# Kernel optimization log

Hardware: AMD Instinct MI355X
Metric: run time of the kernel (lower is better)

## Reference

```python
import jax, jax.numpy as jnp
import numpy as np
import math

BSZ, SEQLEN, DIM = 16, 1, 4096
N_HEADS, N_KV_HEADS = 32, 8
HEAD_DIM = DIM // N_HEADS  # 128
MAX_SEQ_LEN = 4096
START_POS = 4095


def setup_inputs() -> dict:
    key = jax.random.key(0)
    ks = jax.random.split(key, 8)
    w_scale = 0.02
    x = jax.random.normal(ks[0], (1, BSZ, SEQLEN, DIM), jnp.float32)
    wq = jax.random.normal(ks[1], (DIM, DIM), jnp.float32) * w_scale
    wk = jax.random.normal(ks[2], (N_KV_HEADS * HEAD_DIM, DIM), jnp.float32) * w_scale
    wv = jax.random.normal(ks[3], (N_KV_HEADS * HEAD_DIM, DIM), jnp.float32) * w_scale
    wo = jax.random.normal(ks[4], (DIM, DIM), jnp.float32) * w_scale
    cache_k = jax.random.normal(ks[5], (BSZ, MAX_SEQ_LEN, N_KV_HEADS, HEAD_DIM), jnp.float32)
    cache_v = jax.random.normal(ks[6], (BSZ, MAX_SEQ_LEN, N_KV_HEADS, HEAD_DIM), jnp.float32)
    # real RoPE frequencies for positions [START_POS, START_POS+SEQLEN)
    inv_freq = 1.0 / (10000.0 ** (np.arange(0, HEAD_DIM, 2, dtype=np.float32) / HEAD_DIM))
    pos = np.arange(START_POS, START_POS + SEQLEN, dtype=np.float32)
    ang = pos[:, None] * inv_freq[None, :]  # [seqlen, head_dim/2]
    freqs_cos = jnp.asarray(np.cos(ang), jnp.float32)
    freqs_sin = jnp.asarray(np.sin(ang), jnp.float32)
    return {"x": x, "wq": wq, "wk": wk, "wv": wv, "wo": wo,
            "cache_k": cache_k, "cache_v": cache_v,
            "freqs_cos": freqs_cos, "freqs_sin": freqs_sin,
            "start_pos": START_POS}


def _apply_rope(t, cos, sin):
    # t: [b, s, h, d]; cos/sin: [s, d/2]; complex mult over interleaved pairs
    b, s, h, d = t.shape
    tr = t.reshape(b, s, h, d // 2, 2)
    a, bb = tr[..., 0], tr[..., 1]
    c = cos[None, :, None, :]
    sn = sin[None, :, None, :]
    out = jnp.stack([a * c - bb * sn, a * sn + bb * c], axis=-1)
    return out.reshape(b, s, h, d)


def reference(x, wq, wk, wv, wo, cache_k, cache_v, freqs_cos, freqs_sin, start_pos):
    _, bsz, seqlen, dim = x.shape
    n_kv_heads, head_dim = cache_k.shape[2], cache_k.shape[3]
    n_heads = dim // head_dim
    n_rep = n_heads // n_kv_heads

    xq = jnp.einsum('obsd,ed->obse', x, wq).reshape(bsz, seqlen, n_heads, head_dim)
    xk = jnp.einsum('obsd,ed->obse', x, wk).reshape(bsz, seqlen, n_kv_heads, head_dim)
    xv = jnp.einsum('obsd,ed->obse', x, wv).reshape(bsz, seqlen, n_kv_heads, head_dim)

    xq = _apply_rope(xq, freqs_cos, freqs_sin)
    xk = _apply_rope(xk, freqs_cos, freqs_sin)

    cache_k = cache_k.at[:, start_pos:start_pos + seqlen].set(xk)
    cache_v = cache_v.at[:, start_pos:start_pos + seqlen].set(xv)
    keys = cache_k[:, :start_pos + seqlen]    # [b, L, kvh, hd]
    values = cache_v[:, :start_pos + seqlen]

    # repeat_kv (GQA expansion)
    keys = jnp.repeat(keys, n_rep, axis=2)     # [b, L, h, hd]
    values = jnp.repeat(values, n_rep, axis=2)

    scale = 1.0 / math.sqrt(head_dim)
    scores = jnp.einsum('bqhd,bkhd->bhqk', xq, keys) * scale
    # mask is None in decode (seqlen == 1)
    attn = jax.nn.softmax(scores, axis=-1)
    out = jnp.einsum('bhqk,bkhd->bqhd', attn, values)
    out = out.reshape(1, bsz, seqlen, dim)
    return jnp.einsum('obsd,ed->obse', out, wo)
```

## Files before the change

### kernel.cpp

```cpp
#include <hip/hip_runtime.h>
#include <math.h>

#define BSZ 16
#define DIMM 4096
#define NKVH 8
#define HD 128
#define SEQ 4096
#define NSPLIT 8
#define SPLITLEN 512
#define RPAD 65

__device__ __forceinline__ void gemv_rows(const float* __restrict__ xg,
                                          const float* __restrict__ W,
                                          int rbase,
                                          float* __restrict__ x_lds,
                                          float* __restrict__ rbuf,
                                          float res[4], int tid) {
  const int lane = tid & 63;
  float acc[4][16];
#pragma unroll
  for (int r = 0; r < 4; ++r)
#pragma unroll
    for (int b = 0; b < 16; ++b) acc[r][b] = 0.f;

  for (int c = 0; c < 16; ++c) {
    __syncthreads();
#pragma unroll
    for (int u = 0; u < 4; ++u) {
      int f = u * 256 + tid;
      int b = f >> 6;
      int dl = (f & 63) << 2;
      ((float4*)x_lds)[f] = *(const float4*)(xg + (size_t)b * DIMM + c * 256 + dl);
    }
    __syncthreads();
    float4 w4[4];
#pragma unroll
    for (int r = 0; r < 4; ++r)
      w4[r] = *(const float4*)(W + (size_t)(rbase + r) * DIMM + c * 256 + (lane << 2));
#pragma unroll
    for (int b = 0; b < 16; ++b) {
      float4 xv = ((const float4*)x_lds)[b * 64 + lane];
#pragma unroll
      for (int r = 0; r < 4; ++r) {
        acc[r][b] = fmaf(w4[r].x, xv.x, acc[r][b]);
        acc[r][b] = fmaf(w4[r].y, xv.y, acc[r][b]);
        acc[r][b] = fmaf(w4[r].z, xv.z, acc[r][b]);
        acc[r][b] = fmaf(w4[r].w, xv.w, acc[r][b]);
      }
    }
  }
#pragma unroll
  for (int r = 0; r < 4; ++r) {
    __syncthreads();
#pragma unroll
    for (int b = 0; b < 16; ++b) rbuf[b * RPAD + lane] = acc[r][b];
    __syncthreads();
    int bb = lane >> 2, j = lane & 3;
    float s = 0.f;
#pragma unroll
    for (int k = 0; k < 16; ++k) s += rbuf[bb * RPAD + j * 16 + k];
    s += __shfl_xor(s, 1);
    s += __shfl_xor(s, 2);
    res[r] = s;
  }
}

__global__ __launch_bounds__(256) void qkv_kernel(
    const float* __restrict__ x, const float* __restrict__ wq,
    const float* __restrict__ wk, const float* __restrict__ wv,
    const float* __restrict__ fcos, const float* __restrict__ fsin,
    float* __restrict__ q_ws, float* __restrict__ k_ws, float* __restrict__ v_ws) {
  __shared__ float x_lds[4096];
  __shared__ float red[4][16 * RPAD];
  const int tid = threadIdx.x;
  const int lane = tid & 63;
  const int wave = tid >> 6;
  const int row0 = blockIdx.x * 16 + wave * 4;

  const float* W;
  float* outp;
  int rbase, ostride;
  bool rope;
  if (row0 < 4096)      { W = wq; rbase = row0;        outp = q_ws; rope = true;  ostride = 4096; }
  else if (row0 < 5120) { W = wk; rbase = row0 - 4096; outp = k_ws; rope = true;  ostride = 1024; }
  else                  { W = wv; rbase = row0 - 5120; outp = v_ws; rope = false; ostride = 1024; }

  float res[4];
  gemv_rows(x, W, rbase, x_lds, red[wave], res, tid);

  if (rope) {
    int pos = rbase & 127;
#pragma unroll
    for (int r = 0; r < 4; r += 2) {
      int i = (pos + r) >> 1;
      float c = fcos[i], s = fsin[i];
      float a = res[r], b2 = res[r + 1];
      res[r]     = a * c - b2 * s;
      res[r + 1] = a * s + b2 * c;
    }
  }
  if ((lane & 3) == 0) {
    int b = lane >> 2;
#pragma unroll
    for (int r = 0; r < 4; ++r) outp[(size_t)b * ostride + rbase + r] = res[r];
  }
}

__global__ __launch_bounds__(256) void attn_kernel(
    const float* __restrict__ ck, const float* __restrict__ cv,
    const float* __restrict__ q_ws, const float* __restrict__ k_new,
    const float* __restrict__ v_new, float* __restrict__ ml_ws,
    float* __restrict__ opart) {
  __shared__ float sc[SPLITLEN * 4];
  __shared__ float part[16 * 128];
  const int tid = threadIdx.x, lane = tid & 63, wave = tid >> 6;
  const int split = blockIdx.x, kvh = blockIdx.y, b = blockIdx.z;
  const int p0 = split * SPLITLEN;
  const float scale = 0.08838834764831845f;

  const int dsub = (lane & 7) << 2;
  const int prow = lane >> 3;
  float4 q4[4][4];
#pragma unroll
  for (int h = 0; h < 4; ++h)
#pragma unroll
    for (int j = 0; j < 4; ++j) {
      float4 t = *(const float4*)(q_ws + (size_t)b * 4096 + (kvh * 4 + h) * 128 + j * 32 + dsub);
      q4[h][j] = make_float4(t.x * scale, t.y * scale, t.z * scale, t.w * scale);
    }

  for (int it = 0; it < 16; ++it) {
    int p = p0 + wave * 128 + it * 8 + prow;
    const float* kp = (p == 4095) ? (k_new + (size_t)(b * 8 + kvh) * 128)
                                  : (ck + ((size_t)(b * 4096 + p) * 8 + kvh) * 128);
    float s0 = 0, s1 = 0, s2 = 0, s3 = 0;
#pragma unroll
    for (int j = 0; j < 4; ++j) {
      float4 k4 = *(const float4*)(kp + j * 32 + dsub);
      s0 = fmaf(k4.x, q4[0][j].x, s0); s0 = fmaf(k4.y, q4[0][j].y, s0);
      s0 = fmaf(k4.z, q4[0][j].z, s0); s0 = fmaf(k4.w, q4[0][j].w, s0);
      s1 = fmaf(k4.x, q4[1][j].x, s1); s1 = fmaf(k4.y, q4[1][j].y, s1);
      s1 = fmaf(k4.z, q4[1][j].z, s1); s1 = fmaf(k4.w, q4[1][j].w, s1);
      s2 = fmaf(k4.x, q4[2][j].x, s2); s2 = fmaf(k4.y, q4[2][j].y, s2);
      s2 = fmaf(k4.z, q4[2][j].z, s2); s2 = fmaf(k4.w, q4[2][j].w, s2);
      s3 = fmaf(k4.x, q4[3][j].x, s3); s3 = fmaf(k4.y, q4[3][j].y, s3);
      s3 = fmaf(k4.z, q4[3][j].z, s3); s3 = fmaf(k4.w, q4[3][j].w, s3);
    }
#pragma unroll
    for (int m = 1; m <= 4; m <<= 1) {
      s0 += __shfl_xor(s0, m); s1 += __shfl_xor(s1, m);
      s2 += __shfl_xor(s2, m); s3 += __shfl_xor(s3, m);
    }
    if ((lane & 7) == 0)
      ((float4*)sc)[wave * 128 + it * 8 + prow] = make_float4(s0, s1, s2, s3);
  }
  __syncthreads();

  {
    int h = wave;
    float vals[8];
    float m = -1e30f;
#pragma unroll
    for (int k = 0; k < 8; ++k) {
      vals[k] = sc[(k * 64 + lane) * 4 + h];
      m = fmaxf(m, vals[k]);
    }
#pragma unroll
    for (int mk = 1; mk <= 32; mk <<= 1) m = fmaxf(m, __shfl_xor(m, mk));
    float lsum = 0;
#pragma unroll
    for (int k = 0; k < 8; ++k) {
      float e = __expf(vals[k] - m);
      sc[(k * 64 + lane) * 4 + h] = e;
      lsum += e;
    }
#pragma unroll
    for (int mk = 1; mk <= 32; mk <<= 1) lsum += __shfl_xor(lsum, mk);
    if (lane == 0) {
      int hg = kvh * 4 + h;
      ml_ws[((size_t)(b * 32 + hg) * NSPLIT + split) * 2 + 0] = m;
      ml_ws[((size_t)(b * 32 + hg) * NSPLIT + split) * 2 + 1] = lsum;
    }
  }
  __syncthreads();

  {
    int d0 = lane * 2;
    float a00 = 0, a01 = 0, a10 = 0, a11 = 0, a20 = 0, a21 = 0, a30 = 0, a31 = 0;
    for (int k = 0; k < 128; ++k) {
      int pl = wave * 128 + k;
      int p = p0 + pl;
      const float* vp = (p == 4095) ? (v_new + (size_t)(b * 8 + kvh) * 128)
                                    : (cv + ((size_t)(b * 4096 + p) * 8 + kvh) * 128);
      float2 v2 = *(const float2*)(vp + d0);
      float4 s4 = ((const float4*)sc)[pl];
      a00 = fmaf(s4.x, v2.x, a00); a01 = fmaf(s4.x, v2.y, a01);
      a10 = fmaf(s4.y, v2.x, a10); a11 = fmaf(s4.y, v2.y, a11);
      a20 = fmaf(s4.z, v2.x, a20); a21 = fmaf(s4.z, v2.y, a21);
      a30 = fmaf(s4.w, v2.x, a30); a31 = fmaf(s4.w, v2.y, a31);
    }
    *(float2*)&part[(wave * 4 + 0) * 128 + d0] = make_float2(a00, a01);
    *(float2*)&part[(wave * 4 + 1) * 128 + d0] = make_float2(a10, a11);
    *(float2*)&part[(wave * 4 + 2) * 128 + d0] = make_float2(a20, a21);
    *(float2*)&part[(wave * 4 + 3) * 128 + d0] = make_float2(a30, a31);
  }
  __syncthreads();
  {
    int hh = tid >> 6, dd = (tid & 63) * 2;
    float o0 = 0, o1 = 0;
#pragma unroll
    for (int w = 0; w < 4; ++w) {
      o0 += part[(w * 4 + hh) * 128 + dd];
      o1 += part[(w * 4 + hh) * 128 + dd + 1];
    }
    int hg = kvh * 4 + hh;
    size_t base = ((size_t)(b * 32 + hg) * NSPLIT + split) * 128;
    *(float2*)(opart + base + dd) = make_float2(o0, o1);
  }
}

__global__ __launch_bounds__(128) void combine_kernel(
    const float* __restrict__ ml_ws, const float* __restrict__ opart,
    float* __restrict__ attn_ws) {
  int bh = blockIdx.x;
  int d = threadIdx.x;
  float mv[NSPLIT], lv[NSPLIT];
  float M = -1e30f;
#pragma unroll
  for (int i = 0; i < NSPLIT; ++i) {
    mv[i] = ml_ws[((size_t)bh * NSPLIT + i) * 2];
    lv[i] = ml_ws[((size_t)bh * NSPLIT + i) * 2 + 1];
    M = fmaxf(M, mv[i]);
  }
  float L = 0, o = 0;
#pragma unroll
  for (int i = 0; i < NSPLIT; ++i) {
    float w = __expf(mv[i] - M);
    L += w * lv[i];
    o += w * opart[((size_t)bh * NSPLIT + i) * 128 + d];
  }
  attn_ws[(size_t)bh * 128 + d] = o / L;
}

__global__ __launch_bounds__(256) void oproj_kernel(
    const float* __restrict__ xin, const float* __restrict__ wo,
    float* __restrict__ out) {
  __shared__ float x_lds[4096];
  __shared__ float red[4][16 * RPAD];
  const int tid = threadIdx.x;
  const int lane = tid & 63;
  const int wave = tid >> 6;
  const int row0 = blockIdx.x * 16 + wave * 4;
  float res[4];
  gemv_rows(xin, wo, row0, x_lds, red[wave], res, tid);
  if ((lane & 3) == 0) {
    int b = lane >> 2;
#pragma unroll
    for (int r = 0; r < 4; ++r) out[(size_t)b * 4096 + row0 + r] = res[r];
  }
}

extern "C" void kernel_launch(void* const* d_in, const int* in_sizes, int n_in,
                              void* d_out, int out_size, void* d_ws, size_t ws_size,
                              hipStream_t stream) {
  const float* x  = (const float*)d_in[0];
  const float* wq = (const float*)d_in[1];
  const float* wk = (const float*)d_in[2];
  const float* wv = (const float*)d_in[3];
  const float* wo = (const float*)d_in[4];
  const float* ck = (const float*)d_in[5];
  const float* cv = (const float*)d_in[6];
  const float* fc = (const float*)d_in[7];
  const float* fs = (const float*)d_in[8];

  float* ws      = (float*)d_ws;
  float* q_ws    = ws;
  float* k_ws    = q_ws + 65536;
  float* v_ws    = k_ws + 16384;
  float* ml_ws   = v_ws + 16384;
  float* opart   = ml_ws + 8192;
  float* attn_ws = opart + 524288;

  qkv_kernel<<<384, 256, 0, stream>>>(x, wq, wk, wv, fc, fs, q_ws, k_ws, v_ws);
  attn_kernel<<<dim3(NSPLIT, NKVH, BSZ), 256, 0, stream>>>(ck, cv, q_ws, k_ws, v_ws,
                                                           ml_ws, opart);
  combine_kernel<<<BSZ * 32, 128, 0, stream>>>(ml_ws, opart, attn_ws);
  oproj_kernel<<<256, 256, 0, stream>>>(attn_ws, wo, (float*)d_out);
}
```

Baseline: 674.8 us.

## Double grid parallelism in GEMVs and attention splits, write new KV into cache

Halves rows per wave in the QKV and output-projection GEMVs so twice as many blocks run, and doubles the number of KV splits in attention with shorter per-block ranges. The new K/V rows are written directly into the input cache at the last position, removing the per-position branch in the attention loops. The PV accumulation switches to float4 loads over two position halves. This trades more partial results and combine work, plus in-place mutation of input buffers, for higher occupancy and parallelism.

```diff
diff --git a/kernel.cpp b/kernel.cpp
--- a/kernel.cpp
+++ b/kernel.cpp
@@ -6,20 +6,20 @@
 #define NKVH 8
 #define HD 128
 #define SEQ 4096
-#define NSPLIT 8
-#define SPLITLEN 512
+#define NSPLIT 16
+#define SPLITLEN 256
 #define RPAD 65
 
-__device__ __forceinline__ void gemv_rows(const float* __restrict__ xg,
-                                          const float* __restrict__ W,
-                                          int rbase,
-                                          float* __restrict__ x_lds,
-                                          float* __restrict__ rbuf,
-                                          float res[4], int tid) {
+__device__ __forceinline__ void gemv_rows2(const float* __restrict__ xg,
+                                           const float* __restrict__ W,
+                                           int rbase,
+                                           float* __restrict__ x_lds,
+                                           float* __restrict__ rbuf,
+                                           float res[2], int tid) {
   const int lane = tid & 63;
-  float acc[4][16];
-#pragma unroll
-  for (int r = 0; r < 4; ++r)
+  float acc[2][16];
+#pragma unroll
+  for (int r = 0; r < 2; ++r)
 #pragma unroll
     for (int b = 0; b < 16; ++b) acc[r][b] = 0.f;
 
@@ -33,15 +33,15 @@
       ((float4*)x_lds)[f] = *(const float4*)(xg + (size_t)b * DIMM + c * 256 + dl);
     }
     __syncthreads();
-    float4 w4[4];
-#pragma unroll
-    for (int r = 0; r < 4; ++r)
+    float4 w4[2];
+#pragma unroll
+    for (int r = 0; r < 2; ++r)
       w4[r] = *(const float4*)(W + (size_t)(rbase + r) * DIMM + c * 256 + (lane << 2));
 #pragma unroll
     for (int b = 0; b < 16; ++b) {
       float4 xv = ((const float4*)x_lds)[b * 64 + lane];
 #pragma unroll
-      for (int r = 0; r < 4; ++r) {
+      for (int r = 0; r < 2; ++r) {
         acc[r][b] = fmaf(w4[r].x, xv.x, acc[r][b]);
         acc[r][b] = fmaf(w4[r].y, xv.y, acc[r][b]);
         acc[r][b] = fmaf(w4[r].z, xv.z, acc[r][b]);
@@ -50,7 +50,7 @@
     }
   }
 #pragma unroll
-  for (int r = 0; r < 4; ++r) {
+  for (int r = 0; r < 2; ++r) {
     __syncthreads();
 #pragma unroll
     for (int b = 0; b < 16; ++b) rbuf[b * RPAD + lane] = acc[r][b];
@@ -69,99 +69,101 @@
     const float* __restrict__ x, const float* __restrict__ wq,
     const float* __restrict__ wk, const float* __restrict__ wv,
     const float* __restrict__ fcos, const float* __restrict__ fsin,
-    float* __restrict__ q_ws, float* __restrict__ k_ws, float* __restrict__ v_ws) {
+    float* __restrict__ q_ws, float* __restrict__ ckw, float* __restrict__ cvw) {
   __shared__ float x_lds[4096];
   __shared__ float red[4][16 * RPAD];
   const int tid = threadIdx.x;
   const int lane = tid & 63;
   const int wave = tid >> 6;
-  const int row0 = blockIdx.x * 16 + wave * 4;
+  const int row0 = blockIdx.x * 8 + wave * 2;
 
   const float* W;
-  float* outp;
-  int rbase, ostride;
-  bool rope;
-  if (row0 < 4096)      { W = wq; rbase = row0;        outp = q_ws; rope = true;  ostride = 4096; }
-  else if (row0 < 5120) { W = wk; rbase = row0 - 4096; outp = k_ws; rope = true;  ostride = 1024; }
-  else                  { W = wv; rbase = row0 - 5120; outp = v_ws; rope = false; ostride = 1024; }
-
-  float res[4];
-  gemv_rows(x, W, rbase, x_lds, red[wave], res, tid);
-
-  if (rope) {
-    int pos = rbase & 127;
-#pragma unroll
-    for (int r = 0; r < 4; r += 2) {
-      int i = (pos + r) >> 1;
-      float c = fcos[i], s = fsin[i];
-      float a = res[r], b2 = res[r + 1];
-      res[r]     = a * c - b2 * s;
-      res[r + 1] = a * s + b2 * c;
-    }
+  int rbase, kind;
+  if (row0 < 4096)      { W = wq; rbase = row0;        kind = 0; }
+  else if (row0 < 5120) { W = wk; rbase = row0 - 4096; kind = 1; }
+  else                  { W = wv; rbase = row0 - 5120; kind = 2; }
+
+  float res[2];
+  gemv_rows2(x, W, rbase, x_lds, red[wave], res, tid);
+
+  if (kind <= 1) {
+    int i = (rbase & 127) >> 1;
+    float c = fcos[i], s = fsin[i];
+    float a = res[0], b2 = res[1];
+    res[0] = a * c - b2 * s;
+    res[1] = a * s + b2 * c;
   }
   if ((lane & 3) == 0) {
     int b = lane >> 2;
-#pragma unroll
-    for (int r = 0; r < 4; ++r) outp[(size_t)b * ostride + rbase + r] = res[r];
+    if (kind == 0) {
+#pragma unroll
+      for (int r = 0; r < 2; ++r) q_ws[(size_t)b * 4096 + rbase + r] = res[r];
+    } else {
+      int kvh = rbase >> 7, dpos = rbase & 127;
+      float* dst = (kind == 1) ? ckw : cvw;
+#pragma unroll
+      for (int r = 0; r < 2; ++r)
+        dst[((size_t)(b * 4096 + 4095) * 8 + kvh) * 128 + dpos + r] = res[r];
+    }
   }
 }
 
 __global__ __launch_bounds__(256) void attn_kernel(
     const float* __restrict__ ck, const float* __restrict__ cv,
-    const float* __restrict__ q_ws, const float* __restrict__ k_new,
-    const float* __restrict__ v_new, float* __restrict__ ml_ws,
+    const float* __restrict__ q_ws, float* __restrict__ ml_ws,
     float* __restrict__ opart) {
   __shared__ float sc[SPLITLEN * 4];
-  __shared__ float part[16 * 128];
+  __shared__ float part[32 * 128];
   const int tid = threadIdx.x, lane = tid & 63, wave = tid >> 6;
   const int split = blockIdx.x, kvh = blockIdx.y, b = blockIdx.z;
   const int p0 = split * SPLITLEN;
   const float scale = 0.08838834764831845f;
 
-  const int dsub = (lane & 7) << 2;
-  const int prow = lane >> 3;
-  float4 q4[4][4];
-#pragma unroll
-  for (int h = 0; h < 4; ++h)
-#pragma unroll
-    for (int j = 0; j < 4; ++j) {
-      float4 t = *(const float4*)(q_ws + (size_t)b * 4096 + (kvh * 4 + h) * 128 + j * 32 + dsub);
-      q4[h][j] = make_float4(t.x * scale, t.y * scale, t.z * scale, t.w * scale);
-    }
-
-  for (int it = 0; it < 16; ++it) {
-    int p = p0 + wave * 128 + it * 8 + prow;
-    const float* kp = (p == 4095) ? (k_new + (size_t)(b * 8 + kvh) * 128)
-                                  : (ck + ((size_t)(b * 4096 + p) * 8 + kvh) * 128);
-    float s0 = 0, s1 = 0, s2 = 0, s3 = 0;
-#pragma unroll
-    for (int j = 0; j < 4; ++j) {
-      float4 k4 = *(const float4*)(kp + j * 32 + dsub);
-      s0 = fmaf(k4.x, q4[0][j].x, s0); s0 = fmaf(k4.y, q4[0][j].y, s0);
-      s0 = fmaf(k4.z, q4[0][j].z, s0); s0 = fmaf(k4.w, q4[0][j].w, s0);
-      s1 = fmaf(k4.x, q4[1][j].x, s1); s1 = fmaf(k4.y, q4[1][j].y, s1);
-      s1 = fmaf(k4.z, q4[1][j].z, s1); s1 = fmaf(k4.w, q4[1][j].w, s1);
-      s2 = fmaf(k4.x, q4[2][j].x, s2); s2 = fmaf(k4.y, q4[2][j].y, s2);
-      s2 = fmaf(k4.z, q4[2][j].z, s2); s2 = fmaf(k4.w, q4[2][j].w, s2);
-      s3 = fmaf(k4.x, q4[3][j].x, s3); s3 = fmaf(k4.y, q4[3][j].y, s3);
-      s3 = fmaf(k4.z, q4[3][j].z, s3); s3 = fmaf(k4.w, q4[3][j].w, s3);
-    }
-#pragma unroll
-    for (int m = 1; m <= 4; m <<= 1) {
-      s0 += __shfl_xor(s0, m); s1 += __shfl_xor(s1, m);
-      s2 += __shfl_xor(s2, m); s3 += __shfl_xor(s3, m);
-    }
-    if ((lane & 7) == 0)
-      ((float4*)sc)[wave * 128 + it * 8 + prow] = make_float4(s0, s1, s2, s3);
+  {
+    const int dsub = (lane & 7) << 2;
+    const int prow = lane >> 3;
+    float4 q4[4][4];
+#pragma unroll
+    for (int h = 0; h < 4; ++h)
+#pragma unroll
+      for (int j = 0; j < 4; ++j) {
+        float4 t = *(const float4*)(q_ws + (size_t)b * 4096 + (kvh * 4 + h) * 128 + j * 32 + dsub);
+        q4[h][j] = make_float4(t.x * scale, t.y * scale, t.z * scale, t.w * scale);
+      }
+#pragma unroll 2
+    for (int it = 0; it < 8; ++it) {
+      int pl = wave * 64 + it * 8 + prow;
+      const float* kp = ck + ((size_t)(b * 4096 + p0 + pl) * 8 + kvh) * 128;
+      float s0 = 0, s1 = 0, s2 = 0, s3 = 0;
+#pragma unroll
+      for (int j = 0; j < 4; ++j) {
+        float4 k4 = *(const float4*)(kp + j * 32 + dsub);
+        s0 = fmaf(k4.x, q4[0][j].x, s0); s0 = fmaf(k4.y, q4[0][j].y, s0);
+        s0 = fmaf(k4.z, q4[0][j].z, s0); s0 = fmaf(k4.w, q4[0][j].w, s0);
+        s1 = fmaf(k4.x, q4[1][j].x, s1); s1 = fmaf(k4.y, q4[1][j].y, s1);
+        s1 = fmaf(k4.z, q4[1][j].z, s1); s1 = fmaf(k4.w, q4[1][j].w, s1);
+        s2 = fmaf(k4.x, q4[2][j].x, s2); s2 = fmaf(k4.y, q4[2][j].y, s2);
+        s2 = fmaf(k4.z, q4[2][j].z, s2); s2 = fmaf(k4.w, q4[2][j].w, s2);
+        s3 = fmaf(k4.x, q4[3][j].x, s3); s3 = fmaf(k4.y, q4[3][j].y, s3);
+        s3 = fmaf(k4.z, q4[3][j].z, s3); s3 = fmaf(k4.w, q4[3][j].w, s3);
+      }
+#pragma unroll
+      for (int m = 1; m <= 4; m <<= 1) {
+        s0 += __shfl_xor(s0, m); s1 += __shfl_xor(s1, m);
+        s2 += __shfl_xor(s2, m); s3 += __shfl_xor(s3, m);
+      }
+      if ((lane & 7) == 0)
+        ((float4*)sc)[pl] = make_float4(s0, s1, s2, s3);
+    }
   }
   __syncthreads();
 
   {
     int h = wave;
-    float vals[8];
+    float vals[4];
     float m = -1e30f;
 #pragma unroll
-    for (int k = 0; k < 8; ++k) {
+    for (int k = 0; k < 4; ++k) {
       vals[k] = sc[(k * 64 + lane) * 4 + h];
       m = fmaxf(m, vals[k]);
     }
@@ -169,7 +171,7 @@
     for (int mk = 1; mk <= 32; mk <<= 1) m = fmaxf(m, __shfl_xor(m, mk));
     float lsum = 0;
 #pragma unroll
-    for (int k = 0; k < 8; ++k) {
+    for (int k = 0; k < 4; ++k) {
       float e = __expf(vals[k] - m);
       sc[(k * 64 + lane) * 4 + h] = e;
       lsum += e;
@@ -185,33 +187,39 @@
   __syncthreads();
 
   {
-    int d0 = lane * 2;
-    float a00 = 0, a01 = 0, a10 = 0, a11 = 0, a20 = 0, a21 = 0, a30 = 0, a31 = 0;
-    for (int k = 0; k < 128; ++k) {
-      int pl = wave * 128 + k;
-      int p = p0 + pl;
-      const float* vp = (p == 4095) ? (v_new + (size_t)(b * 8 + kvh) * 128)
-                                    : (cv + ((size_t)(b * 4096 + p) * 8 + kvh) * 128);
-      float2 v2 = *(const float2*)(vp + d0);
+    const int dq = lane & 31;
+    const int half = lane >> 5;
+    float4 a0 = {0,0,0,0}, a1 = {0,0,0,0}, a2 = {0,0,0,0}, a3 = {0,0,0,0};
+#pragma unroll 4
+    for (int it = 0; it < 32; ++it) {
+      int pl = wave * 64 + it * 2 + half;
+      const float* vp = cv + ((size_t)(b * 4096 + p0 + pl) * 8 + kvh) * 128;
+      float4 v4 = *(const float4*)(vp + dq * 4);
       float4 s4 = ((const float4*)sc)[pl];
-      a00 = fmaf(s4.x, v2.x, a00); a01 = fmaf(s4.x, v2.y, a01);
-      a10 = fmaf(s4.y, v2.x, a10); a11 = fmaf(s4.y, v2.y, a11);
-      a20 = fmaf(s4.z, v2.x, a20); a21 = fmaf(s4.z, v2.y, a21);
-      a30 = fmaf(s4.w, v2.x, a30); a31 = fmaf(s4.w, v2.y, a31);
-    }
-    *(float2*)&part[(wave * 4 + 0) * 128 + d0] = make_float2(a00, a01);
-    *(float2*)&part[(wave * 4 + 1) * 128 + d0] = make_float2(a10, a11);
-    *(float2*)&part[(wave * 4 + 2) * 128 + d0] = make_float2(a20, a21);
-    *(float2*)&part[(wave * 4 + 3) * 128 + d0] = make_float2(a30, a31);
+      a0.x = fmaf(s4.x, v4.x, a0.x); a0.y = fmaf(s4.x, v4.y, a0.y);
+      a0.z = fmaf(s4.x, v4.z, a0.z); a0.w = fmaf(s4.x, v4.w, a0.w);
+      a1.x = fmaf(s4.y, v4.x, a1.x); a1.y = fmaf(s4.y, v4.y, a1.y);
+      a1.z = fmaf(s4.y, v4.z, a1.z); a1.w = fmaf(s4.y, v4.w, a1.w);
+      a2.x = fmaf(s4.z, v4.x, a2.x); a2.y = fmaf(s4.z, v4.y, a2.y);
+      a2.z = fmaf(s4.z, v4.z, a2.z); a2.w = fmaf(s4.z, v4.w, a2.w);
+      a3.x = fmaf(s4.w, v4.x, a3.x); a3.y = fmaf(s4.w, v4.y, a3.y);
+      a3.z = fmaf(s4.w, v4.z, a3.z); a3.w = fmaf(s4.w, v4.w, a3.w);
+    }
+    int rb = (half * 16 + wave * 4) * 128 + dq * 4;
+    *(float4*)&part[rb + 0 * 128] = a0;
+    *(float4*)&part[rb + 1 * 128] = a1;
+    *(float4*)&part[rb + 2 * 128] = a2;
+    *(float4*)&part[rb + 3 * 128] = a3;
   }
   __syncthreads();
   {
     int hh = tid >> 6, dd = (tid & 63) * 2;
     float o0 = 0, o1 = 0;
 #pragma unroll
-    for (int w = 0; w < 4; ++w) {
-      o0 += part[(w * 4 + hh) * 128 + dd];
-      o1 += part[(w * 4 + hh) * 128 + dd + 1];
+    for (int g = 0; g < 8; ++g) {
+      int row = (g >> 2) * 16 + (g & 3) * 4 + hh;
+      float2 p2 = *(const float2*)&part[row * 128 + dd];
+      o0 += p2.x; o1 += p2.y;
     }
     int hg = kvh * 4 + hh;
     size_t base = ((size_t)(b * 32 + hg) * NSPLIT + split) * 128;
@@ -250,13 +258,13 @@
   const int tid = threadIdx.x;
   const int lane = tid & 63;
   const int wave = tid >> 6;
-  const int row0 = blockIdx.x * 16 + wave * 4;
-  float res[4];
-  gemv_rows(xin, wo, row0, x_lds, red[wave], res, tid);
+  const int row0 = blockIdx.x * 8 + wave * 2;
+  float res[2];
+  gemv_rows2(xin, wo, row0, x_lds, red[wave], res, tid);
   if ((lane & 3) == 0) {
     int b = lane >> 2;
 #pragma unroll
-    for (int r = 0; r < 4; ++r) out[(size_t)b * 4096 + row0 + r] = res[r];
+    for (int r = 0; r < 2; ++r) out[(size_t)b * 4096 + row0 + r] = res[r];
   }
 }
 
@@ -268,22 +276,19 @@
   const float* wk = (const float*)d_in[2];
   const float* wv = (const float*)d_in[3];
   const float* wo = (const float*)d_in[4];
-  const float* ck = (const float*)d_in[5];
-  const float* cv = (const float*)d_in[6];
+  float* ck = (float*)d_in[5];
+  float* cv = (float*)d_in[6];
   const float* fc = (const float*)d_in[7];
   const float* fs = (const float*)d_in[8];
 
   float* ws      = (float*)d_ws;
   float* q_ws    = ws;
-  float* k_ws    = q_ws + 65536;
-  float* v_ws    = k_ws + 16384;
-  float* ml_ws   = v_ws + 16384;
-  float* opart   = ml_ws + 8192;
-  float* attn_ws = opart + 524288;
-
-  qkv_kernel<<<384, 256, 0, stream>>>(x, wq, wk, wv, fc, fs, q_ws, k_ws, v_ws);
-  attn_kernel<<<dim3(NSPLIT, NKVH, BSZ), 256, 0, stream>>>(ck, cv, q_ws, k_ws, v_ws,
-                                                           ml_ws, opart);
+  float* ml_ws   = q_ws + 65536;
+  float* opart   = ml_ws + 16384;
+  float* attn_ws = opart + 1048576;
+
+  qkv_kernel<<<768, 256, 0, stream>>>(x, wq, wk, wv, fc, fs, q_ws, ck, cv);
+  attn_kernel<<<dim3(NSPLIT, NKVH, BSZ), 256, 0, stream>>>(ck, cv, q_ws, ml_ws, opart);
   combine_kernel<<<BSZ * 32, 128, 0, stream>>>(ml_ws, opart, attn_ws);
-  oproj_kernel<<<256, 256, 0, stream>>>(attn_ws, wo, (float*)d_out);
-}
+  oproj_kernel<<<512, 256, 0, stream>>>(attn_ws, wo, (float*)d_out);
+}
```

New measurement: 661.5 us. -2.0%, faster.
